# Kernel optimization log

Hardware: AMD Instinct MI355X
Metric: run time of the kernel (lower is better)

The kernel has to match this reference:

```python
import jax, jax.numpy as jnp
import numpy as np

D_MODEL = 1024
NUM_HEADS = 16
D_K = D_MODEL // NUM_HEADS
MAX_LEN = 1024
BATCH = 8
SEQ = 1024


def setup_inputs() -> dict:
    key = jax.random.key(0)
    ks = jax.random.split(key, 12)
    s = 0.02
    inp = {
        "x": jax.random.normal(ks[0], (BATCH, SEQ, D_MODEL), dtype=jnp.float32),
        "Wq": jax.random.normal(ks[1], (D_MODEL, D_MODEL), dtype=jnp.float32) * s,
        "bq": jnp.zeros((D_MODEL,), dtype=jnp.float32),
        "Wk": jax.random.normal(ks[2], (D_MODEL, D_MODEL), dtype=jnp.float32) * s,
        "bk": jnp.zeros((D_MODEL,), dtype=jnp.float32),
        "Wv": jax.random.normal(ks[3], (D_MODEL, D_MODEL), dtype=jnp.float32) * s,
        "bv": jnp.zeros((D_MODEL,), dtype=jnp.float32),
        "Wo": jax.random.normal(ks[4], (D_MODEL, D_MODEL), dtype=jnp.float32) * s,
        "bo": jnp.zeros((D_MODEL,), dtype=jnp.float32),
        "relative_k": jax.random.normal(ks[5], (2 * MAX_LEN - 1, D_K), dtype=jnp.float32),
        "relative_v": jax.random.normal(ks[6], (2 * MAX_LEN - 1, D_K), dtype=jnp.float32),
    }
    return inp


def reference(x, Wq, bq, Wk, bk, Wv, bv, Wo, bo, relative_k, relative_v):
    B, L, D = x.shape
    H, dk = NUM_HEADS, D_K
    # projections (nn.Linear: y = x @ W.T + b), split into heads -> [B,H,L,dk]
    Q = (x @ Wq.T + bq).reshape(B, L, H, dk).transpose(0, 2, 1, 3)
    K = (x @ Wk.T + bk).reshape(B, L, H, dk).transpose(0, 2, 1, 3)
    V = (x @ Wv.T + bv).reshape(B, L, H, dk).transpose(0, 2, 1, 3)
    # relative position index table: rel_pos[l, r] = r - l + max_len - 1
    rel_pos = jnp.arange(L)[None, :] - jnp.arange(L)[:, None] + (MAX_LEN - 1)
    rel_k = relative_k[rel_pos]  # [L, L, dk]
    rel_v = relative_v[rel_pos]  # [L, L, dk]
    scale = 1.0 / np.sqrt(dk).astype(np.float32)
    scores = jnp.einsum('bhld,bhrd->bhlr', Q, K) * scale
    scores = scores + jnp.einsum('bhld,lrd->bhlr', Q, rel_k)
    attn = jax.nn.softmax(scores, axis=-1)  # [B,H,L,L]
    out = jnp.einsum('bhlr,bhrd->bhld', attn, V)
    out = out + jnp.einsum('bhlr,lrd->bhld', attn, rel_v)
    out = out.transpose(0, 2, 1, 3).reshape(B, L, D)
    return out @ Wo.T + bo
```

## Files before the change

### kernel.cpp

```cpp
#include <hip/hip_runtime.h>

typedef _Float16 f16;
typedef _Float16 f16x2 __attribute__((ext_vector_type(2)));
typedef _Float16 f16x8 __attribute__((ext_vector_type(8)));
typedef float f32x4 __attribute__((ext_vector_type(4)));

static __device__ __forceinline__ f32x4 mfma16(f16x8 a, f16x8 b, f32x4 c) {
  return __builtin_amdgcn_mfma_f32_16x16x32_f16(a, b, c, 0, 0, 0);
}

#define GL16(GP, LP)                                                         \
  __builtin_amdgcn_global_load_lds(                                          \
      (const __attribute__((address_space(1))) void*)(GP),                   \
      (__attribute__((address_space(3))) void*)(LP), 16, 0, 0)

__global__ void pack_f16_kernel(const float* __restrict__ s, f16* __restrict__ d, int n) {
  int i = blockIdx.x * 256 + threadIdx.x;
  if (i < n) d[i] = (f16)s[i];
}

__global__ void pack_relk_kernel(const float* __restrict__ relk, f16* __restrict__ dst) {
  int idx = blockIdx.x * 256 + threadIdx.x;
  dst[idx] = (idx < 2047 * 64) ? (f16)relk[idx] : (f16)0.f;
}

__global__ void pack_relvt_kernel(const float* __restrict__ relv, f16* __restrict__ dst) {
  int idx = blockIdx.x * 256 + threadIdx.x;
  int dd = idx >> 11, p = idx & 2047;
  dst[idx] = (p < 2047) ? (f16)relv[p * 64 + dd] : (f16)0.f;
}

template <int OUT_F32, int BIAS_ROW>
__global__ __launch_bounds__(256, 2) void gemm_bt(
    const f16* __restrict__ A, const f16* __restrict__ B,
    const float* __restrict__ bias, void* __restrict__ Cout,
    int M, int N, int Kd, float oscale) {
  __shared__ __align__(16) f16 Al[128 * 64];
  __shared__ __align__(16) f16 Bl[128 * 64];
  const int tid = threadIdx.x;
  const int w = tid >> 6, lane = tid & 63;
  const int l15 = lane & 15, hi = lane >> 4;
  const long i0 = (long)blockIdx.y * 128, j0 = (long)blockIdx.x * 128;
  const int wr = (w >> 1) * 64, wc = (w & 1) * 64;
  const int sx = (l15 & 7) * 8;

  const int row_in = lane >> 3, c_lds = lane & 7;
  const int cg8 = (c_lds ^ row_in) * 8;
  const f16* agl = A + (i0 + w * 8 + row_in) * Kd + cg8;
  const f16* bgl = B + (j0 + w * 8 + row_in) * Kd + cg8;

  f32x4 acc[4][4];
#pragma unroll
  for (int a = 0; a < 4; a++)
#pragma unroll
    for (int b2 = 0; b2 < 4; b2++) acc[a][b2] = (f32x4){0.f, 0.f, 0.f, 0.f};

  for (int k0 = 0; k0 < Kd; k0 += 64) {
    __syncthreads();
#pragma unroll
    for (int s = 0; s < 4; s++) {
      GL16(agl + (long)s * 32 * Kd + k0, Al + (s * 32 + w * 8) * 64);
      GL16(bgl + (long)s * 32 * Kd + k0, Bl + (s * 32 + w * 8) * 64);
    }
    __syncthreads();
#pragma unroll
    for (int ks = 0; ks < 2; ks++) {
      f16x8 af[4], bf[4];
#pragma unroll
      for (int mb = 0; mb < 4; mb++)
        af[mb] = *(const f16x8*)&Al[(wr + mb * 16 + l15) * 64 + ((ks * 32 + hi * 8) ^ sx)];
#pragma unroll
      for (int nb = 0; nb < 4; nb++)
        bf[nb] = *(const f16x8*)&Bl[(wc + nb * 16 + l15) * 64 + ((ks * 32 + hi * 8) ^ sx)];
#pragma unroll
      for (int mb = 0; mb < 4; mb++)
#pragma unroll
        for (int nb = 0; nb < 4; nb++) acc[mb][nb] = mfma16(af[mb], bf[nb], acc[mb][nb]);
    }
  }
#pragma unroll
  for (int mb = 0; mb < 4; mb++) {
#pragma unroll
    for (int nb = 0; nb < 4; nb++) {
      long row = i0 + wr + mb * 16 + hi * 4;
      long col = j0 + wc + nb * 16 + l15;
      float bc = BIAS_ROW ? 0.f : bias[col];
#pragma unroll
      for (int i = 0; i < 4; i++) {
        float v = acc[mb][nb][i] + (BIAS_ROW ? bias[row + i] : bc);
        v *= oscale;
        if (OUT_F32)
          ((float*)Cout)[(row + i) * N + col] = v;
        else
          ((f16*)Cout)[(row + i) * N + col] = (f16)v;
      }
    }
  }
}

__global__ __launch_bounds__(256, 2) void attn_kernel(
    const f16* __restrict__ Qh, const f16* __restrict__ Kh,
    const f16* __restrict__ Vth, const f16* __restrict__ relKh,
    const f16* __restrict__ relVTh, f16* __restrict__ AO) {
  __shared__ __align__(16) f16 SH[38912];
  f16* const ldsK = SH;
  f16* const ldsRK = SH + 4096;
  f16* const ldsP = SH;
  f16* const ldsPS = SH + 9216;
  f16* const ldsV = SH + 22528;
  f16* const ldsRV = SH + 26624;

  const int tid = threadIdx.x;
  const int w = tid >> 6, lane = tid & 63;
  const int l15 = lane & 15, hi = lane >> 4;
  const int flat = blockIdx.x;
  const int xcd = flat & 7, slot = flat >> 3;
  const int bh = xcd * 16 + (slot >> 3);
  const int qt = slot & 7;
  const int b = bh >> 4, h = bh & 15;
  const int l0 = qt * 128;
  const int cu = 6 - 2 * w;
  const int rvco = 96 - 32 * w;
  const int sx = (l15 & 7) * 8;

  const int row_in = lane >> 3;
  const int c_lds = lane & 7;
  const int cg8 = (c_lds ^ row_in) * 8;
  const f16* kgl = Kh + ((long)(b * 1024 + w * 16 + row_in)) * 1024 + h * 64 + cg8;
  const f16* vgl = Vth + ((long)(h * 64 + w * 16 + row_in)) * 8192 + b * 1024 + cg8;
  const f16* rkgl = relKh + (long)(896 - l0 + w * 48 + row_in) * 64 + cg8;
#define RVP(Q)                                                                   \
  (relVTh + (long)(((w * 6 + (Q)) * 64 + lane) / 24) * 2048 + (896 - l0) +       \
   ((((w * 6 + (Q)) * 64 + lane) % 24) ^ ((((w * 6 + (Q)) * 64 + lane) / 24) & 7)) * 8)
  const f16* rvg0 = RVP(0);
  const f16* rvg1 = RVP(1);
  const f16* rvg2 = RVP(2);
  const f16* rvg3 = RVP(3);
  const f16* rvg4 = RVP(4);
  const f16* rvg5 = RVP(5);
#undef RVP

  const long qbase = ((long)(b * 1024 + l0 + w * 32 + l15)) * 1024 + h * 64 + hi * 8;
  const f16x8 qf00 = *(const f16x8*)(Qh + qbase);
  const f16x8 qf01 = *(const f16x8*)(Qh + qbase + 32);
  const f16x8 qf10 = *(const f16x8*)(Qh + qbase + 16l * 1024);
  const f16x8 qf11 = *(const f16x8*)(Qh + qbase + 16l * 1024 + 32);

  const f16x8 ones1 = {(f16)1.f, (f16)1.f, (f16)1.f, (f16)1.f,
                       (f16)1.f, (f16)1.f, (f16)1.f, (f16)1.f};

  f32x4 acc_o[2][4];
#pragma unroll
  for (int g = 0; g < 2; g++)
#pragma unroll
    for (int cf = 0; cf < 4; cf++) acc_o[g][cf] = (f32x4){0.f, 0.f, 0.f, 0.f};
  float mrow[2][4], lsum[2][4];
#pragma unroll
  for (int g = 0; g < 2; g++)
#pragma unroll
    for (int i = 0; i < 4; i++) {
      mrow[g][i] = -1e30f;
      lsum[g][i] = 0.f;
    }

  for (int kt = 0; kt < 16; kt++) {
    const int r0 = kt * 64;
    __syncthreads();
    {
      const long ko = (long)r0 * 1024;
      GL16(kgl + ko, ldsK + (w * 16) * 64);
      GL16(kgl + ko + 8 * 1024, ldsK + (w * 16 + 8) * 64);
      GL16(vgl + r0, ldsV + (w * 16) * 64);
      GL16(vgl + r0 + 8l * 8192, ldsV + (w * 16 + 8) * 64);
      const int rko = r0 * 64;
      GL16(rkgl + rko, ldsRK + (w * 48) * 64);
      GL16(rkgl + rko + 512, ldsRK + (w * 48 + 8) * 64);
      GL16(rkgl + rko + 1024, ldsRK + (w * 48 + 16) * 64);
      GL16(rkgl + rko + 1536, ldsRK + (w * 48 + 24) * 64);
      GL16(rkgl + rko + 2048, ldsRK + (w * 48 + 32) * 64);
      GL16(rkgl + rko + 2560, ldsRK + (w * 48 + 40) * 64);
      GL16(rvg0 + r0, ldsRV + (w * 6 + 0) * 512);
      GL16(rvg1 + r0, ldsRV + (w * 6 + 1) * 512);
      GL16(rvg2 + r0, ldsRV + (w * 6 + 2) * 512);
      GL16(rvg3 + r0, ldsRV + (w * 6 + 3) * 512);
      GL16(rvg4 + r0, ldsRV + (w * 6 + 4) * 512);
      GL16(rvg5 + r0, ldsRV + (w * 6 + 5) * 512);
    }
    __syncthreads();

    f32x4 sacc[2][4], qracc[2][5];
#pragma unroll
    for (int g = 0; g < 2; g++) {
#pragma unroll
      for (int cf = 0; cf < 4; cf++) sacc[g][cf] = (f32x4){0.f, 0.f, 0.f, 0.f};
#pragma unroll
      for (int j = 0; j < 5; j++) qracc[g][j] = (f32x4){0.f, 0.f, 0.f, 0.f};
    }
    __builtin_amdgcn_s_setprio(1);
#pragma unroll
    for (int ks = 0; ks < 2; ks++) {
      f16x8 kf[4], rf[6];
#pragma unroll
      for (int cf = 0; cf < 4; cf++)
        kf[cf] = *(const f16x8*)&ldsK[(cf * 16 + l15) * 64 + ((ks * 32 + hi * 8) ^ sx)];
#pragma unroll
      for (int j = 0; j < 6; j++)
        rf[j] =
            *(const f16x8*)&ldsRK[((cu + j) * 16 + l15) * 64 + ((ks * 32 + hi * 8) ^ sx)];
      f16x8 q0 = ks ? qf01 : qf00;
      f16x8 q1 = ks ? qf11 : qf10;
#pragma unroll
      for (int cf = 0; cf < 4; cf++) {
        sacc[0][cf] = mfma16(q0, kf[cf], sacc[0][cf]);
        sacc[1][cf] = mfma16(q1, kf[cf], sacc[1][cf]);
      }
#pragma unroll
      for (int j = 0; j < 5; j++) {
        qracc[0][j] = mfma16(q0, rf[j + 1], qracc[0][j]);
        qracc[1][j] = mfma16(q1, rf[j], qracc[1][j]);
      }
    }
    __builtin_amdgcn_s_setprio(0);
    __syncthreads();

#pragma unroll
    for (int g = 0; g < 2; g++)
#pragma unroll
      for (int i = 0; i < 4; i++) {
        int t = 15 + l15 - (hi * 4 + i);
        int idx = (hi * 16 + (t & 15)) * 4;
        bool wrap = t >= 16;
#pragma unroll
        for (int cf = 0; cf < 4; cf++) {
          auto pkv = __builtin_amdgcn_cvt_pkrtz(qracc[g][cf][i], qracc[g][cf + 1][i]);
          int gg = __builtin_amdgcn_ds_bpermute(idx, __builtin_bit_cast(int, pkv));
          f16x2 two = __builtin_bit_cast(f16x2, gg);
          sacc[g][cf][i] += (float)(wrap ? two[1] : two[0]);
        }
      }

    float rmax[2][4];
#pragma unroll
    for (int g = 0; g < 2; g++)
#pragma unroll
      for (int i = 0; i < 4; i++)
        rmax[g][i] = fmaxf(fmaxf(sacc[g][0][i], sacc[g][1][i]),
                           fmaxf(sacc[g][2][i], sacc[g][3][i]));
#pragma unroll
    for (int m = 1; m < 16; m <<= 1)
#pragma unroll
      for (int g = 0; g < 2; g++)
#pragma unroll
        for (int i = 0; i < 4; i++)
          rmax[g][i] = fmaxf(rmax[g][i], __shfl_xor(rmax[g][i], m, 64));
    {
      bool big = false;
#pragma unroll
      for (int g = 0; g < 2; g++)
#pragma unroll
        for (int i = 0; i < 4; i++) big |= rmax[g][i] > mrow[g][i] + 8.f;
      if (__any(big)) {
#pragma unroll
        for (int g = 0; g < 2; g++)
#pragma unroll
          for (int i = 0; i < 4; i++) {
            float mn = fmaxf(mrow[g][i], rmax[g][i]);
            float al = __expf(mrow[g][i] - mn);
            mrow[g][i] = mn;
            lsum[g][i] *= al;
#pragma unroll
            for (int cf = 0; cf < 4; cf++) acc_o[g][cf][i] *= al;
          }
      }
    }
#pragma unroll
    for (int g = 0; g < 2; g++)
#pragma unroll
      for (int cf = 0; cf < 4; cf++)
#pragma unroll
        for (int i = 0; i < 4; i++)
          sacc[g][cf][i] = __expf(sacc[g][cf][i] - mrow[g][i]);

    const uint4 z4 = make_uint4(0u, 0u, 0u, 0u);
#pragma unroll
    for (int r2 = 0; r2 < 2; r2++)
#pragma unroll
      for (int s = 0; s < 3; s++)
        *(uint4*)&ldsPS[(w * 32 + r2 * 16 + (lane >> 2)) * 104 + (lane & 3) * 8 + 32 * s] =
            z4;
#pragma unroll
    for (int g = 0; g < 2; g++)
#pragma unroll
      for (int cf = 0; cf < 4; cf++)
#pragma unroll
        for (int i = 0; i < 4; i++) {
          int rr = 16 * g + hi * 4 + i;
          int ri = cf * 16 + l15;
          f16 ph = (f16)sacc[g][cf][i];
          ldsP[(w * 32 + rr) * 72 + ri] = ph;
          ldsPS[(w * 32 + rr) * 104 + 31 + ri - rr] = ph;
        }
    asm volatile("s_waitcnt lgkmcnt(0)" ::: "memory");

    __builtin_amdgcn_s_setprio(1);
    f32x4 rs0 = (f32x4){0.f, 0.f, 0.f, 0.f}, rs1 = (f32x4){0.f, 0.f, 0.f, 0.f};
#pragma unroll
    for (int ks = 0; ks < 2; ks++) {
      f16x8 pa0 = *(const f16x8*)&ldsP[(w * 32 + l15) * 72 + ks * 32 + hi * 8];
      f16x8 pa1 = *(const f16x8*)&ldsP[(w * 32 + 16 + l15) * 72 + ks * 32 + hi * 8];
      rs0 = mfma16(pa0, ones1, rs0);
      rs1 = mfma16(pa1, ones1, rs1);
#pragma unroll
      for (int cf = 0; cf < 4; cf++) {
        f16x8 vb = *(const f16x8*)&ldsV[(cf * 16 + l15) * 64 + ((ks * 32 + hi * 8) ^ sx)];
        acc_o[0][cf] = mfma16(pa0, vb, acc_o[0][cf]);
        acc_o[1][cf] = mfma16(pa1, vb, acc_o[1][cf]);
      }
    }
#pragma unroll
    for (int ks = 0; ks < 3; ks++) {
      f16x8 ps0 = *(const f16x8*)&ldsPS[(w * 32 + l15) * 104 + ks * 32 + hi * 8];
      f16x8 ps1 = *(const f16x8*)&ldsPS[(w * 32 + 16 + l15) * 104 + ks * 32 + hi * 8];
#pragma unroll
      for (int cf = 0; cf < 4; cf++) {
        f16x8 rb = *(const f16x8*)&ldsRV[(cf * 16 + l15) * 192 +
                                         ((rvco + ks * 32 + hi * 8) ^ sx)];
        acc_o[0][cf] = mfma16(ps0, rb, acc_o[0][cf]);
        acc_o[1][cf] = mfma16(ps1, rb, acc_o[1][cf]);
      }
    }
    __builtin_amdgcn_s_setprio(0);
#pragma unroll
    for (int i = 0; i < 4; i++) {
      lsum[0][i] += rs0[i];
      lsum[1][i] += rs1[i];
    }
  }
#pragma unroll
  for (int g = 0; g < 2; g++)
#pragma unroll
    for (int cf = 0; cf < 4; cf++)
#pragma unroll
      for (int i = 0; i < 4; i++) {
        float v = acc_o[g][cf][i] / lsum[g][i];
        AO[((long)(b * 1024 + l0 + w * 32 + 16 * g + hi * 4 + i)) * 1024 + h * 64 +
           cf * 16 + l15] = (f16)v;
      }
}

extern "C" void kernel_launch(void* const* d_in, const int* in_sizes, int n_in,
                              void* d_out, int out_size, void* d_ws, size_t ws_size,
                              hipStream_t stream) {
  const float* x = (const float*)d_in[0];
  const float* Wq = (const float*)d_in[1];
  const float* bq = (const float*)d_in[2];
  const float* Wk = (const float*)d_in[3];
  const float* bk = (const float*)d_in[4];
  const float* Wv = (const float*)d_in[5];
  const float* bv = (const float*)d_in[6];
  const float* Wo = (const float*)d_in[7];
  const float* bo = (const float*)d_in[8];
  const float* relk = (const float*)d_in[9];
  const float* relv = (const float*)d_in[10];
  float* out = (float*)d_out;

  char* ws = (char*)d_ws;
  size_t off = 0;
  auto alloc = [&](size_t bytes) {
    char* p = ws + off;
    off += (bytes + 255) & ~(size_t)255;
    return p;
  };
  f16* xh = (f16*)alloc(8192ull * 1024 * 2);
  f16* Wqh = (f16*)alloc(1024ull * 1024 * 2);
  f16* Wkh = (f16*)alloc(1024ull * 1024 * 2);
  f16* Wvh = (f16*)alloc(1024ull * 1024 * 2);
  f16* Woh = (f16*)alloc(1024ull * 1024 * 2);
  f16* relKh = (f16*)alloc(2048ull * 64 * 2);
  f16* relVTh = (f16*)alloc(64ull * 2048 * 2);
  f16* Qh = (f16*)alloc(8192ull * 1024 * 2);
  f16* Kh = (f16*)alloc(8192ull * 1024 * 2);
  f16* Vth = (f16*)alloc(1024ull * 8192 * 2);
  f16* AOh = (f16*)alloc(8192ull * 1024 * 2);
  if (ws_size < off) return;

  pack_f16_kernel<<<32768, 256, 0, stream>>>(x, xh, 8192 * 1024);
  pack_f16_kernel<<<4096, 256, 0, stream>>>(Wq, Wqh, 1024 * 1024);
  pack_f16_kernel<<<4096, 256, 0, stream>>>(Wk, Wkh, 1024 * 1024);
  pack_f16_kernel<<<4096, 256, 0, stream>>>(Wv, Wvh, 1024 * 1024);
  pack_f16_kernel<<<4096, 256, 0, stream>>>(Wo, Woh, 1024 * 1024);
  pack_relk_kernel<<<512, 256, 0, stream>>>(relk, relKh);
  pack_relvt_kernel<<<512, 256, 0, stream>>>(relv, relVTh);

  dim3 g1(8, 64);
  gemm_bt<0, 0><<<g1, 256, 0, stream>>>(xh, Wqh, bq, Qh, 8192, 1024, 1024, 1.0f);
  gemm_bt<0, 0><<<g1, 256, 0, stream>>>(xh, Wkh, bk, Kh, 8192, 1024, 1024, 0.125f);
  dim3 g2(64, 8);
  gemm_bt<0, 1><<<g2, 256, 0, stream>>>(Wvh, xh, bv, Vth, 1024, 8192, 1024, 1.0f);

  attn_kernel<<<1024, 256, 0, stream>>>(Qh, Kh, Vth, relKh, relVTh, AOh);

  gemm_bt<1, 0><<<g1, 256, 0, stream>>>(AOh, Woh, bo, out, 8192, 1024, 1024, 1.0f);
}
```

Baseline: 304.2 us.

## Double-buffer LDS tiles in projection GEMM to overlap loads with MFMA

The projection GEMM now uses two LDS buffers per operand and issues async global-to-LDS loads for the next K tile before computing on the current one. Partial vmcnt waits and raw s_barrier replace the two __syncthreads per iteration. LDS use per block doubles, to 64 KB, which may limit occupancy at two blocks per CU. Separately, in the attention kernel an explicit lgkmcnt(0) wait after the P stores becomes a sched_barrier, relying on compiler-inserted waits.

```diff
diff --git a/kernel.cpp b/kernel.cpp
--- a/kernel.cpp
+++ b/kernel.cpp
@@ -35,8 +35,8 @@
     const f16* __restrict__ A, const f16* __restrict__ B,
     const float* __restrict__ bias, void* __restrict__ Cout,
     int M, int N, int Kd, float oscale) {
-  __shared__ __align__(16) f16 Al[128 * 64];
-  __shared__ __align__(16) f16 Bl[128 * 64];
+  __shared__ __align__(16) f16 Al[2 * 128 * 64];
+  __shared__ __align__(16) f16 Bl[2 * 128 * 64];
   const int tid = threadIdx.x;
   const int w = tid >> 6, lane = tid & 63;
   const int l15 = lane & 15, hi = lane >> 4;
@@ -48,6 +48,21 @@
   const int cg8 = (c_lds ^ row_in) * 8;
   const f16* agl = A + (i0 + w * 8 + row_in) * Kd + cg8;
   const f16* bgl = B + (j0 + w * 8 + row_in) * Kd + cg8;
+  const int lbase = (w * 8) * 64;
+
+#define GSTAGE(BUF, K0)                                          \
+  do {                                                           \
+    f16* al = Al + (BUF) * 8192 + lbase;                         \
+    f16* bl = Bl + (BUF) * 8192 + lbase;                         \
+    GL16(agl + (K0), al);                                        \
+    GL16(agl + 32l * Kd + (K0), al + 32 * 64);                   \
+    GL16(agl + 64l * Kd + (K0), al + 64 * 64);                   \
+    GL16(agl + 96l * Kd + (K0), al + 96 * 64);                   \
+    GL16(bgl + (K0), bl);                                        \
+    GL16(bgl + 32l * Kd + (K0), bl + 32 * 64);                   \
+    GL16(bgl + 64l * Kd + (K0), bl + 64 * 64);                   \
+    GL16(bgl + 96l * Kd + (K0), bl + 96 * 64);                   \
+  } while (0)
 
   f32x4 acc[4][4];
 #pragma unroll
@@ -55,29 +70,38 @@
 #pragma unroll
     for (int b2 = 0; b2 < 4; b2++) acc[a][b2] = (f32x4){0.f, 0.f, 0.f, 0.f};
 
+  GSTAGE(0, 0);
+  int cur = 0;
   for (int k0 = 0; k0 < Kd; k0 += 64) {
-    __syncthreads();
-#pragma unroll
-    for (int s = 0; s < 4; s++) {
-      GL16(agl + (long)s * 32 * Kd + k0, Al + (s * 32 + w * 8) * 64);
-      GL16(bgl + (long)s * 32 * Kd + k0, Bl + (s * 32 + w * 8) * 64);
-    }
-    __syncthreads();
+    if (k0 + 64 < Kd) {
+      GSTAGE(cur ^ 1, k0 + 64);
+      asm volatile("s_waitcnt vmcnt(8)" ::: "memory");
+    } else {
+      asm volatile("s_waitcnt vmcnt(0)" ::: "memory");
+    }
+    __builtin_amdgcn_s_barrier();
+    __builtin_amdgcn_sched_barrier(0);
+    const f16* Ac = Al + cur * 8192;
+    const f16* Bc = Bl + cur * 8192;
 #pragma unroll
     for (int ks = 0; ks < 2; ks++) {
       f16x8 af[4], bf[4];
 #pragma unroll
       for (int mb = 0; mb < 4; mb++)
-        af[mb] = *(const f16x8*)&Al[(wr + mb * 16 + l15) * 64 + ((ks * 32 + hi * 8) ^ sx)];
+        af[mb] = *(const f16x8*)&Ac[(wr + mb * 16 + l15) * 64 + ((ks * 32 + hi * 8) ^ sx)];
 #pragma unroll
       for (int nb = 0; nb < 4; nb++)
-        bf[nb] = *(const f16x8*)&Bl[(wc + nb * 16 + l15) * 64 + ((ks * 32 + hi * 8) ^ sx)];
+        bf[nb] = *(const f16x8*)&Bc[(wc + nb * 16 + l15) * 64 + ((ks * 32 + hi * 8) ^ sx)];
 #pragma unroll
       for (int mb = 0; mb < 4; mb++)
 #pragma unroll
         for (int nb = 0; nb < 4; nb++) acc[mb][nb] = mfma16(af[mb], bf[nb], acc[mb][nb]);
     }
+    asm volatile("s_waitcnt lgkmcnt(0)" ::: "memory");
+    __builtin_amdgcn_s_barrier();
+    cur ^= 1;
   }
+#undef GSTAGE
 #pragma unroll
   for (int mb = 0; mb < 4; mb++) {
 #pragma unroll
@@ -300,7 +324,7 @@
           ldsP[(w * 32 + rr) * 72 + ri] = ph;
           ldsPS[(w * 32 + rr) * 104 + 31 + ri - rr] = ph;
         }
-    asm volatile("s_waitcnt lgkmcnt(0)" ::: "memory");
+    __builtin_amdgcn_sched_barrier(0);
 
     __builtin_amdgcn_s_setprio(1);
     f32x4 rs0 = (f32x4){0.f, 0.f, 0.f, 0.f}, rs1 = (f32x4){0.f, 0.f, 0.f, 0.f};
```

Result: no change. 300.1 us (-1.3%).
